# Performance work log

Measured on AMD Instinct MI355X. Metric: run time of the kernel, lower is better.

## Reference

```python
import jax, jax.numpy as jnp
import numpy as np
import itertools

B, K, H, W = 64, 5, 320, 320
EPS = 1e-6
# All K! permutations (exact equivalent of scipy.linear_sum_assignment for KxK cost)
PERMS = np.array(list(itertools.permutations(range(K))), dtype=np.int32)  # [P, K]


def setup_inputs() -> dict:
    key = jax.random.key(0)
    k1, k2, k3 = jax.random.split(key, 3)
    return {
        "fg_logits": jax.random.normal(k1, (B, 1, H, W), dtype=jnp.float32),
        "slot_logits": jax.random.normal(k2, (B, K, H, W), dtype=jnp.float32),
        "target": jax.random.uniform(k3, (B, 1, H, W), dtype=jnp.float32),
    }


def reference(fg_logits, slot_logits, target):
    fg = target[:, 0]            # [B,H,W]
    bg = 1.0 - fg                # [B,H,W]
    # targets_b: index 0 = FG mask, 1..K-1 = BG mask (duplicated)  -> [B,K,H,W]
    targets = jnp.concatenate([fg[:, None], jnp.broadcast_to(bg[:, None], (B, K - 1, H, W))], axis=1)

    # IoU cost matrix on detached sigmoid probs (matches .detach())
    probs = jax.lax.stop_gradient(jax.nn.sigmoid(slot_logits))
    s = probs.reshape(B, K, -1)        # [B,K,N]
    t = targets.reshape(B, K, -1)      # [B,K,N]
    inter = jnp.einsum('bkn,bjn->bkj', s, t)           # [B,K,K]
    union = s.sum(-1)[:, :, None] + t.sum(-1)[:, None, :] - inter + EPS
    cost = 1.0 - inter / union                          # [B,K,K]

    # Exact Hungarian via brute force over K! permutations (K small)
    perms = jnp.asarray(PERMS)                          # [P,K]
    rows = jnp.arange(K)[None, :]                       # [1,K]
    perm_cost = cost[:, rows, perms].sum(-1)            # [B,P]
    best_perm = perms[jnp.argmin(perm_cost, axis=1)]    # [B,K] col_ind per sample

    # aligned[i] = targets[col_ind[i]]; targets[j] is fg iff j == 0
    is_fg = (best_perm == 0)[:, :, None, None]          # [B,K,1,1]
    aligned = jnp.where(is_fg, fg[:, None], bg[:, None])  # [B,K,H,W]

    # Stable sigmoid-BCE with logits, mean-reduced per sample then averaged over B
    x = slot_logits
    bce = jnp.maximum(x, 0.0) - x * aligned + jnp.log1p(jnp.exp(-jnp.abs(x)))
    return bce.mean()
```

## Files before the change

kernel.cpp:

```cpp
#include <hip/hip_runtime.h>


#define BB 64
#define KK 5
#define NPIX 102400
#define QUARTERS 4
#define SEG 25600
#define ITERS 25
#define THREADS 256
#define REC 8
#define NBLK (BB * KK * QUARTERS)

__global__ void hung_pass1(const float* __restrict__ slot,
                           const float* __restrict__ tgt,
                           float* __restrict__ ws)
{
    const int bid = blockIdx.x;
    const int q   = bid & (QUARTERS - 1);
    const int bk  = bid >> 2;
    const int b   = bk / KK;

    const float* xk = slot + (size_t)bk * NPIX + q * SEG;
    const float* t  = tgt  + (size_t)b  * NPIX + q * SEG;

    float X = 0.f, XF = 0.f, S = 0.f, SF = 0.f, PX = 0.f, Tf = 0.f;

    const int base = threadIdx.x * 4;
    #pragma unroll 5
    for (int i = 0; i < ITERS; ++i) {
        const int off = base + i * (THREADS * 4);
        const float4 fg4 = *reinterpret_cast<const float4*>(t  + off);
        const float4 x4  = *reinterpret_cast<const float4*>(xk + off);
        const float fgv[4] = {fg4.x, fg4.y, fg4.z, fg4.w};
        const float xv[4]  = {x4.x, x4.y, x4.z, x4.w};
        #pragma unroll
        for (int j = 0; j < 4; ++j) {
            const float x  = xv[j];
            const float fg = fgv[j];
            const float e  = __expf(-fabsf(x));
            const float L  = __logf(1.0f + e);
            const float d  = L + fmaxf(-x, 0.0f);
            const float s  = __expf(-d);
            PX += d;
            X  += x;
            XF  = fmaf(x, fg, XF);
            S  += s;
            SF  = fmaf(s, fg, SF);
            Tf += fg;
        }
    }

    float v[6] = {X, XF, S, SF, PX, Tf};
    #pragma unroll
    for (int j = 0; j < 6; ++j) {
        float x = v[j];
        #pragma unroll
        for (int off = 32; off > 0; off >>= 1) x += __shfl_down(x, off, 64);
        v[j] = x;
    }
    __shared__ float red[THREADS / 64][6];
    const int lane = threadIdx.x & 63;
    const int w    = threadIdx.x >> 6;
    if (lane == 0) {
        #pragma unroll
        for (int j = 0; j < 6; ++j) red[w][j] = v[j];
    }
    __syncthreads();
    if (threadIdx.x < 6) {
        const int j = threadIdx.x;
        ws[(size_t)bid * REC + j] =
            red[0][j] + red[1][j] + red[2][j] + red[3][j];
    }
}

__global__ __launch_bounds__(320) void hung_pass2(const float* __restrict__ ws,
                                                  float* __restrict__ out)
{
    __shared__ float red[BB][KK][6];
    const int t = threadIdx.x;
    if (t < BB * KK) {
        float v[6] = {0, 0, 0, 0, 0, 0};
        #pragma unroll
        for (int q = 0; q < QUARTERS; ++q) {
            const float* p = ws + (size_t)(t * QUARTERS + q) * REC;
            #pragma unroll
            for (int j = 0; j < 6; ++j) v[j] += p[j];
        }
        const int b = t / KK, k = t - b * KK;
        #pragma unroll
        for (int j = 0; j < 6; ++j) red[b][k][j] = v[j];
    }
    __syncthreads();
    if (t < BB) {
        const int b = t;
        const float Tf = red[b][0][5];
        const float Tb = (float)NPIX - Tf;
        float best = 3.402823466e+38f; int kb = 0;
        float xfsum = 0.f, px = 0.f;
        #pragma unroll
        for (int k = 0; k < KK; ++k) {
            const float Sv = red[b][k][2], Iv = red[b][k][3];
            const float cf = 1.f - Iv / (Sv + Tf - Iv + 1e-6f);
            const float Ib = Sv - Iv;
            const float cb = 1.f - Ib / (Sv + Tb - Ib + 1e-6f);
            const float dd = cf - cb;
            if (dd < best) { best = dd; kb = k; }
            xfsum += red[b][k][1];
            px    += red[b][k][4];
        }
        float res = px + xfsum - (2.f * red[b][kb][1] - red[b][kb][0]);
        #pragma unroll
        for (int off = 32; off > 0; off >>= 1) res += __shfl_down(res, off, 64);
        if (b == 0) out[0] = res * (1.0f / 32768000.0f);
    }
}

extern "C" void kernel_launch(void* const* d_in, const int* in_sizes, int n_in,
                              void* d_out, int out_size, void* d_ws, size_t ws_size,
                              hipStream_t stream) {
    const float* slot = (const float*)d_in[1];
    const float* tgt  = (const float*)d_in[2];
    float* out = (float*)d_out;
    float* ws  = (float*)d_ws;

    hung_pass1<<<NBLK, THREADS, 0, stream>>>(slot, tgt, ws);
    hung_pass2<<<1, 320, 0, stream>>>(ws, out);
}
```

Before: 223.3 us.

## Process all slots per block to reuse target loads, use nontemporal loads

Each block now covers one batch sample and one of 20 pixel segments and walks all 5 slot channels, so each target pixel is loaded once instead of five times. Loads are marked nontemporal and the loop is fully unrolled. The cost is 26 accumulators per thread plus wider reductions, which raises register pressure and reduction overhead. Pass 2 now also does a longer 20-segment gather per (b,k).

```diff
diff --git a/kernel.cpp b/kernel.cpp
--- a/kernel.cpp
+++ b/kernel.cpp
@@ -4,72 +4,94 @@
 #define BB 64
 #define KK 5
 #define NPIX 102400
-#define QUARTERS 4
-#define SEG 25600
-#define ITERS 25
+#define Q 20
+#define SEG (NPIX / Q)
 #define THREADS 256
-#define REC 8
-#define NBLK (BB * KK * QUARTERS)
+#define ITERS (SEG / (THREADS * 4))
+#define REC 32
+#define NVAL 26
+#define NBLK (BB * Q)
+
+typedef float f4 __attribute__((ext_vector_type(4)));
 
 __global__ void hung_pass1(const float* __restrict__ slot,
                            const float* __restrict__ tgt,
                            float* __restrict__ ws)
 {
     const int bid = blockIdx.x;
-    const int q   = bid & (QUARTERS - 1);
-    const int bk  = bid >> 2;
-    const int b   = bk / KK;
+    const int b   = bid / Q;
+    const int q   = bid - b * Q;
 
-    const float* xk = slot + (size_t)bk * NPIX + q * SEG;
-    const float* t  = tgt  + (size_t)b  * NPIX + q * SEG;
+    const float* sb = slot + (size_t)b * KK * NPIX + q * SEG;
+    const float* t  = tgt  + (size_t)b * NPIX      + q * SEG;
 
-    float X = 0.f, XF = 0.f, S = 0.f, SF = 0.f, PX = 0.f, Tf = 0.f;
+    float aX[KK]  = {0,0,0,0,0};
+    float aXF[KK] = {0,0,0,0,0};
+    float aS[KK]  = {0,0,0,0,0};
+    float aSF[KK] = {0,0,0,0,0};
+    float aPX[KK] = {0,0,0,0,0};
+    float Tf = 0.f;
 
     const int base = threadIdx.x * 4;
-    #pragma unroll 5
+    #pragma unroll
     for (int i = 0; i < ITERS; ++i) {
         const int off = base + i * (THREADS * 4);
-        const float4 fg4 = *reinterpret_cast<const float4*>(t  + off);
-        const float4 x4  = *reinterpret_cast<const float4*>(xk + off);
-        const float fgv[4] = {fg4.x, fg4.y, fg4.z, fg4.w};
-        const float xv[4]  = {x4.x, x4.y, x4.z, x4.w};
+        const f4 fg4 = __builtin_nontemporal_load(
+            reinterpret_cast<const f4*>(t + off));
+        f4 x4[KK];
         #pragma unroll
-        for (int j = 0; j < 4; ++j) {
-            const float x  = xv[j];
-            const float fg = fgv[j];
-            const float e  = __expf(-fabsf(x));
-            const float L  = __logf(1.0f + e);
-            const float d  = L + fmaxf(-x, 0.0f);
-            const float s  = __expf(-d);
-            PX += d;
-            X  += x;
-            XF  = fmaf(x, fg, XF);
-            S  += s;
-            SF  = fmaf(s, fg, SF);
-            Tf += fg;
+        for (int k = 0; k < KK; ++k)
+            x4[k] = __builtin_nontemporal_load(
+                reinterpret_cast<const f4*>(sb + (size_t)k * NPIX + off));
+
+        Tf += (fg4.x + fg4.y) + (fg4.z + fg4.w);
+
+        #pragma unroll
+        for (int k = 0; k < KK; ++k) {
+            #pragma unroll
+            for (int j = 0; j < 4; ++j) {
+                const float x  = x4[k][j];
+                const float fg = fg4[j];
+                const float e  = __expf(-fabsf(x));
+                const float L  = __logf(1.0f + e);
+                const float d  = L + fmaxf(-x, 0.0f);
+                const float s  = __expf(-d);
+                aPX[k] += d;
+                aX[k]  += x;
+                aXF[k]  = fmaf(x, fg, aXF[k]);
+                aS[k]  += s;
+                aSF[k]  = fmaf(s, fg, aSF[k]);
+            }
         }
     }
 
-    float v[6] = {X, XF, S, SF, PX, Tf};
+    float v[NVAL];
     #pragma unroll
-    for (int j = 0; j < 6; ++j) {
-        float x = v[j];
+    for (int k = 0; k < KK; ++k) {
+        v[k*5+0] = aX[k];  v[k*5+1] = aXF[k]; v[k*5+2] = aS[k];
+        v[k*5+3] = aSF[k]; v[k*5+4] = aPX[k];
+    }
+    v[25] = Tf;
+
+    #pragma unroll
+    for (int jv = 0; jv < NVAL; ++jv) {
+        float x = v[jv];
         #pragma unroll
         for (int off = 32; off > 0; off >>= 1) x += __shfl_down(x, off, 64);
-        v[j] = x;
+        v[jv] = x;
     }
-    __shared__ float red[THREADS / 64][6];
+    __shared__ float red[THREADS / 64][NVAL];
     const int lane = threadIdx.x & 63;
     const int w    = threadIdx.x >> 6;
     if (lane == 0) {
         #pragma unroll
-        for (int j = 0; j < 6; ++j) red[w][j] = v[j];
+        for (int jv = 0; jv < NVAL; ++jv) red[w][jv] = v[jv];
     }
     __syncthreads();
-    if (threadIdx.x < 6) {
-        const int j = threadIdx.x;
-        ws[(size_t)bid * REC + j] =
-            red[0][j] + red[1][j] + red[2][j] + red[3][j];
+    if (threadIdx.x < NVAL) {
+        const int jv = threadIdx.x;
+        ws[(size_t)bid * REC + jv] =
+            red[0][jv] + red[1][jv] + red[2][jv] + red[3][jv];
     }
 }
 
@@ -78,17 +100,19 @@
 {
     __shared__ float red[BB][KK][6];
     const int t = threadIdx.x;
-    if (t < BB * KK) {
-        float v[6] = {0, 0, 0, 0, 0, 0};
+    {
+        const int b = t / KK, k = t - (t / KK) * KK;
+        float v[5] = {0, 0, 0, 0, 0};
+        float tf = 0.f;
+        for (int q = 0; q < Q; ++q) {
+            const float* p = ws + (size_t)(b * Q + q) * REC;
+            #pragma unroll
+            for (int c = 0; c < 5; ++c) v[c] += p[k * 5 + c];
+            if (k == 0) tf += p[25];
+        }
         #pragma unroll
-        for (int q = 0; q < QUARTERS; ++q) {
-            const float* p = ws + (size_t)(t * QUARTERS + q) * REC;
-            #pragma unroll
-            for (int j = 0; j < 6; ++j) v[j] += p[j];
-        }
-        const int b = t / KK, k = t - b * KK;
-        #pragma unroll
-        for (int j = 0; j < 6; ++j) red[b][k][j] = v[j];
+        for (int c = 0; c < 5; ++c) red[b][k][c] = v[c];
+        if (k == 0) red[b][0][5] = tf;
     }
     __syncthreads();
     if (t < BB) {
```

Result: no change. 221.0 us (-1.0%).
